# Kernel tuning notes

Hardware: AMD Instinct MI355X
Metric: run time of the kernel (lower is better)

Reference implementation:

```python
import jax, jax.numpy as jnp
import numpy as np
from jax import lax

M_RANGE = 1  # padding = m_range, kernel is (2*m_range+1)^2 = 9 classes of 3x3


def _conv(x, kernel):
    # torch F.conv2d (cross-correlation), stride 1, padding M_RANGE
    return lax.conv_general_dilated(
        x, kernel, window_strides=(1, 1),
        padding=[(M_RANGE, M_RANGE), (M_RANGE, M_RANGE)],
        dimension_numbers=('NCHW', 'OIHW', 'NCHW'))


def _construct_seg(ones, m_mask, m_kernel):
    # ones.expand_as(m_mask) * m_mask, then per-sample conv2d -> batched conv
    return _conv(ones * m_mask, m_kernel)  # [B,1,H,W]


def _construct_image(im, m_mask, appear, m_kernel):
    # im: [B,C,H,W]; m_mask: [B,K,H,W]; appear: [B,1,H,W]
    im = im * appear
    B, C, H, W = im.shape
    K = m_mask.shape[1]
    # fuse the python double loop: fold (B,C) into batch, conv K->1 once
    im_expand = (im[:, :, None, :, :] * m_mask[:, None, :, :, :]).reshape(B * C, K, H, W)
    return _conv(im_expand, m_kernel).reshape(B, C, H, W)


def setup_inputs() -> dict:
    key = jax.random.key(0)
    k0, k1, k2, k3 = jax.random.split(key, 4)
    B, C, H, W, K, N_INPUTS = 32, 3, 256, 256, 9, 2
    im_input_f = jax.random.uniform(k0, (B, N_INPUTS * C, H, W), dtype=jnp.float32)
    im_input_b = jax.random.uniform(k1, (B, N_INPUTS * C, H, W), dtype=jnp.float32)
    ones = jnp.ones((B, 1, H, W), dtype=jnp.float32)
    # gt motion masks: soft per-pixel distribution over K motion classes
    gt_motion_f = jax.nn.softmax(jax.random.normal(k2, (B, K, H, W), dtype=jnp.float32), axis=1)
    gt_motion_b = jax.nn.softmax(jax.random.normal(k3, (B, K, H, W), dtype=jnp.float32), axis=1)
    # one-hot displacement kernels: kernel i has a 1 at flat position i of the 3x3 window
    m_kernel = jnp.eye(K, dtype=jnp.float32).reshape(K, 3, 3)[None]  # [1,K,3,3]
    return {"im_input_f": im_input_f, "im_input_b": im_input_b, "ones": ones,
            "gt_motion_f": gt_motion_f, "gt_motion_b": gt_motion_b, "m_kernel": m_kernel}


def reference(im_input_f, im_input_b, ones, gt_motion_f, gt_motion_b, m_kernel):
    IM_CHANNEL = 3
    relu = jax.nn.relu
    m_mask_f, m_mask_b = gt_motion_f, gt_motion_b

    seg_f = _construct_seg(ones, m_mask_f, m_kernel)
    seg_b = _construct_seg(ones, m_mask_b, m_kernel)

    disappear_f = relu(seg_f - 1)
    appear_f = relu(1 - disappear_f)
    disappear_b = relu(seg_b - 1)
    appear_b = relu(1 - disappear_b)

    pred_f = _construct_image(im_input_f[:, -IM_CHANNEL:, :, :], m_mask_f, appear_f, m_kernel)
    pred_b = _construct_image(im_input_b[:, -IM_CHANNEL:, :, :], m_mask_b, appear_b, m_kernel)

    seg_f = 1 - relu(1 - seg_f)
    seg_b = 1 - relu(1 - seg_b)
    attn = (seg_f + 1e-5) / (seg_f + seg_b + 2e-5)  # [B,1,H,W], broadcasts over C
    pred = attn * pred_f + (1 - attn) * pred_b
    return (pred, m_mask_f, 1 - appear_f, attn, m_mask_b, 1 - appear_b, 1 - attn)
```

## Files before the change

### kernel.cpp

```cpp
#include <hip/hip_runtime.h>

#define BB 32
#define KK 9
#define CC 3
#define HH 256
#define WW 256
#define HW (HH * WW)

#define SZ_P ((size_t)BB * CC * HW)
#define SZ_M ((size_t)BB * KK * HW)
#define SZ_S ((size_t)BB * HW)

#define TX 64
#define TY 16
#define TILES_X (WW / TX)
#define TILES_Y (HH / TY)
#define TILES_PER_B (TILES_X * TILES_Y)

__global__ __launch_bounds__(256) void fused_binet_kernel(
    const float* __restrict__ im_f, const float* __restrict__ im_b,
    const float* __restrict__ gt_f, const float* __restrict__ gt_b,
    float* __restrict__ out) {
  __shared__ float s_sf[TY + 2][TX + 2];
  __shared__ float s_sb[TY + 2][TX + 2];

  int bid = blockIdx.x;
  int b = bid / TILES_PER_B;
  int t = bid % TILES_PER_B;
  int ty0 = (t / TILES_X) * TY;
  int tx0 = (t % TILES_X) * TX;

  const float* gf  = gt_f + (size_t)b * KK * HW;
  const float* gb  = gt_b + (size_t)b * KK * HW;
  const float* imf = im_f + ((size_t)b * 6 + 3) * HW;
  const float* imb = im_b + ((size_t)b * 6 + 3) * HW;

  int tid = threadIdx.x;

  for (int i = tid; i < (TY + 2) * (TX + 2); i += 256) {
    int ly = i / (TX + 2);
    int lx = i - ly * (TX + 2);
    int y = ty0 + ly - 1;
    int x = tx0 + lx - 1;
    float sf = 0.f, sb = 0.f;
    if (y >= 0 && y < HH && x >= 0 && x < WW) {
#pragma unroll
      for (int k = 0; k < KK; ++k) {
        int yy = y + (k / 3) - 1;
        int xx = x + (k % 3) - 1;
        if (yy >= 0 && yy < HH && xx >= 0 && xx < WW) {
          int off = k * HW + (yy << 8) + xx;
          sf += gf[off];
          sb += gb[off];
        }
      }
    }
    s_sf[ly][lx] = sf;
    s_sb[ly][lx] = sb;
  }
  __syncthreads();

  float* o_mf     = out + SZ_P;
  float* o_disf   = out + SZ_P + SZ_M;
  float* o_attn   = o_disf + SZ_S;
  float* o_mb     = o_attn + SZ_S;
  float* o_disb   = o_mb + SZ_M;
  float* o_1mattn = o_disb + SZ_S;

  int lx  = tid & (TX - 1);
  int ly0 = tid >> 6;

#pragma unroll
  for (int r = 0; r < 4; ++r) {
    int ly = ly0 + r * 4;
    int h = ty0 + ly;
    int w = tx0 + lx;
    int hw = (h << 8) + w;
    size_t sidx = (size_t)b * HW + hw;

    float sf = s_sf[ly + 1][lx + 1];
    float sb = s_sb[ly + 1][lx + 1];
    float dis_f = fmaxf(sf - 1.f, 0.f);
    float app_f = fmaxf(1.f - dis_f, 0.f);
    float dis_b = fmaxf(sb - 1.f, 0.f);
    float app_b = fmaxf(1.f - dis_b, 0.f);
    float sfc = 1.f - fmaxf(1.f - sf, 0.f);
    float sbc = 1.f - fmaxf(1.f - sb, 0.f);
    float attn = (sfc + 1e-5f) / (sfc + sbc + 2e-5f);

    o_disf[sidx]   = 1.f - app_f;
    o_attn[sidx]   = attn;
    o_disb[sidx]   = 1.f - app_b;
    o_1mattn[sidx] = 1.f - attn;

    float pf0 = 0.f, pf1 = 0.f, pf2 = 0.f;
    float pb0 = 0.f, pb1 = 0.f, pb2 = 0.f;
#pragma unroll
    for (int k = 0; k < KK; ++k) {
      size_t moff = (size_t)b * KK * HW + (size_t)k * HW + hw;
      o_mf[moff] = gf[k * HW + hw];
      o_mb[moff] = gb[k * HW + hw];

      int y = h + (k / 3) - 1;
      int x = w + (k % 3) - 1;
      if (y >= 0 && y < HH && x >= 0 && x < WW) {
        int p = (y << 8) + x;
        float sfq = s_sf[ly + (k / 3)][lx + (k % 3)];
        float af = fmaxf(1.f - fmaxf(sfq - 1.f, 0.f), 0.f);
        float cf = af * gf[k * HW + p];
        pf0 = fmaf(cf, imf[p], pf0);
        pf1 = fmaf(cf, imf[HW + p], pf1);
        pf2 = fmaf(cf, imf[2 * HW + p], pf2);
        float sbq = s_sb[ly + (k / 3)][lx + (k % 3)];
        float ab = fmaxf(1.f - fmaxf(sbq - 1.f, 0.f), 0.f);
        float cb = ab * gb[k * HW + p];
        pb0 = fmaf(cb, imb[p], pb0);
        pb1 = fmaf(cb, imb[HW + p], pb1);
        pb2 = fmaf(cb, imb[2 * HW + p], pb2);
      }
    }
    float at2 = 1.f - attn;
    size_t pbase = (size_t)b * CC * HW + hw;
    out[pbase]          = fmaf(attn, pf0, at2 * pb0);
    out[pbase + HW]     = fmaf(attn, pf1, at2 * pb1);
    out[pbase + 2 * HW] = fmaf(attn, pf2, at2 * pb2);
  }
}

extern "C" void kernel_launch(void* const* d_in, const int* in_sizes, int n_in,
                              void* d_out, int out_size, void* d_ws, size_t ws_size,
                              hipStream_t stream) {
  const float* im_f = (const float*)d_in[0];
  const float* im_b = (const float*)d_in[1];
  const float* gt_f = (const float*)d_in[3];
  const float* gt_b = (const float*)d_in[4];
  float* out = (float*)d_out;

  dim3 block(256);
  dim3 grid(BB * TILES_PER_B);

  fused_binet_kernel<<<grid, block, 0, stream>>>(im_f, im_b, gt_f, gt_b, out);
}
```

Before: 458.0 us.

## Compute seg in registers per pixel, halo-only ring pass, swizzle block order

Each thread now loads the 9 shifted mask values for its own pixels once, keeps them in registers to form the seg sum and later reuse it for the image prediction, and writes the interior of the shared seg tile directly. A separate pass computes only the halo ring. Block size goes to 512 threads with 2 rows per thread, and block indices are remapped with an XCD-style swizzle so neighbouring tiles share L2. The aim is to cut the redundant gathers of the mask tensor, at the cost of higher register pressure from the 36 kept values.

Measured after the change: 421.0 us. 1.09x faster.

```diff
diff --git a/kernel.cpp b/kernel.cpp
--- a/kernel.cpp
+++ b/kernel.cpp
@@ -13,11 +13,9 @@
 
 #define TX 64
 #define TY 16
-#define TILES_X (WW / TX)
-#define TILES_Y (HH / TY)
-#define TILES_PER_B (TILES_X * TILES_Y)
+#define RING ((TY + 2) * (TX + 2) - TY * TX)
 
-__global__ __launch_bounds__(256) void fused_binet_kernel(
+__global__ __launch_bounds__(512) void fused_binet_kernel(
     const float* __restrict__ im_f, const float* __restrict__ im_b,
     const float* __restrict__ gt_f, const float* __restrict__ gt_b,
     float* __restrict__ out) {
@@ -25,40 +23,16 @@
   __shared__ float s_sb[TY + 2][TX + 2];
 
   int bid = blockIdx.x;
-  int b = bid / TILES_PER_B;
-  int t = bid % TILES_PER_B;
-  int ty0 = (t / TILES_X) * TY;
-  int tx0 = (t % TILES_X) * TX;
+  int actual = ((bid & 7) << 8) | (bid >> 3);
+  int b   = actual >> 6;
+  int rem = actual & 63;
+  int tx0 = (rem >> 4) << 6;
+  int ty0 = (rem & 15) << 4;
 
   const float* gf  = gt_f + (size_t)b * KK * HW;
   const float* gb  = gt_b + (size_t)b * KK * HW;
   const float* imf = im_f + ((size_t)b * 6 + 3) * HW;
   const float* imb = im_b + ((size_t)b * 6 + 3) * HW;
-
-  int tid = threadIdx.x;
-
-  for (int i = tid; i < (TY + 2) * (TX + 2); i += 256) {
-    int ly = i / (TX + 2);
-    int lx = i - ly * (TX + 2);
-    int y = ty0 + ly - 1;
-    int x = tx0 + lx - 1;
-    float sf = 0.f, sb = 0.f;
-    if (y >= 0 && y < HH && x >= 0 && x < WW) {
-#pragma unroll
-      for (int k = 0; k < KK; ++k) {
-        int yy = y + (k / 3) - 1;
-        int xx = x + (k % 3) - 1;
-        if (yy >= 0 && yy < HH && xx >= 0 && xx < WW) {
-          int off = k * HW + (yy << 8) + xx;
-          sf += gf[off];
-          sb += gb[off];
-        }
-      }
-    }
-    s_sf[ly][lx] = sf;
-    s_sb[ly][lx] = sb;
-  }
-  __syncthreads();
 
   float* o_mf     = out + SZ_P;
   float* o_disf   = out + SZ_P + SZ_M;
@@ -67,19 +41,83 @@
   float* o_disb   = o_mb + SZ_M;
   float* o_1mattn = o_disb + SZ_S;
 
+  int tid = threadIdx.x;
   int lx  = tid & (TX - 1);
   int ly0 = tid >> 6;
 
+  float rf[2][KK], rb[2][KK];
+  float segf[2], segb[2];
+
 #pragma unroll
-  for (int r = 0; r < 4; ++r) {
-    int ly = ly0 + r * 4;
-    int h = ty0 + ly;
-    int w = tx0 + lx;
-    int hw = (h << 8) + w;
+  for (int r = 0; r < 2; ++r) {
+    int ly = ly0 + r * 8;
+    int h  = ty0 + ly;
+    int w  = tx0 + lx;
+    int hw = (h << 8) | w;
+    float sf = 0.f, sb = 0.f;
+#pragma unroll
+    for (int k = 0; k < KK; ++k) {
+      int y = h + (k / 3) - 1;
+      int x = w + (k % 3) - 1;
+      float vf = 0.f, vb = 0.f;
+      if ((unsigned)y < HH && (unsigned)x < WW) {
+        int p = k * HW + (y << 8) + x;
+        vf = gf[p];
+        vb = gb[p];
+      }
+      rf[r][k] = vf;
+      rb[r][k] = vb;
+      sf += vf;
+      sb += vb;
+      size_t moff = (size_t)b * KK * HW + (size_t)k * HW + hw;
+      o_mf[moff] = gf[k * HW + hw];
+      o_mb[moff] = gb[k * HW + hw];
+    }
+    segf[r] = sf;
+    segb[r] = sb;
+    s_sf[ly + 1][lx + 1] = sf;
+    s_sb[ly + 1][lx + 1] = sb;
+  }
+
+  if (tid < RING) {
+    int ly, lxr;
+    if (tid < TX + 2) { ly = 0; lxr = tid; }
+    else if (tid < 2 * (TX + 2)) { ly = TY + 1; lxr = tid - (TX + 2); }
+    else {
+      int j = tid - 2 * (TX + 2);
+      ly  = 1 + (j & 15);
+      lxr = (j >> 4) ? (TX + 1) : 0;
+    }
+    int yq = ty0 + ly - 1;
+    int xq = tx0 + lxr - 1;
+    float sf = 0.f, sb = 0.f;
+    if ((unsigned)yq < HH && (unsigned)xq < WW) {
+#pragma unroll
+      for (int k = 0; k < KK; ++k) {
+        int y = yq + (k / 3) - 1;
+        int x = xq + (k % 3) - 1;
+        if ((unsigned)y < HH && (unsigned)x < WW) {
+          int p = k * HW + (y << 8) + x;
+          sf += gf[p];
+          sb += gb[p];
+        }
+      }
+    }
+    s_sf[ly][lxr] = sf;
+    s_sb[ly][lxr] = sb;
+  }
+  __syncthreads();
+
+#pragma unroll
+  for (int r = 0; r < 2; ++r) {
+    int ly = ly0 + r * 8;
+    int h  = ty0 + ly;
+    int w  = tx0 + lx;
+    int hw = (h << 8) | w;
     size_t sidx = (size_t)b * HW + hw;
 
-    float sf = s_sf[ly + 1][lx + 1];
-    float sb = s_sb[ly + 1][lx + 1];
+    float sf = segf[r];
+    float sb = segb[r];
     float dis_f = fmaxf(sf - 1.f, 0.f);
     float app_f = fmaxf(1.f - dis_f, 0.f);
     float dis_b = fmaxf(sb - 1.f, 0.f);
@@ -97,23 +135,20 @@
     float pb0 = 0.f, pb1 = 0.f, pb2 = 0.f;
 #pragma unroll
     for (int k = 0; k < KK; ++k) {
-      size_t moff = (size_t)b * KK * HW + (size_t)k * HW + hw;
-      o_mf[moff] = gf[k * HW + hw];
-      o_mb[moff] = gb[k * HW + hw];
-
-      int y = h + (k / 3) - 1;
-      int x = w + (k % 3) - 1;
-      if (y >= 0 && y < HH && x >= 0 && x < WW) {
+      int dy = k / 3, dx = k % 3;
+      int y = h + dy - 1;
+      int x = w + dx - 1;
+      if ((unsigned)y < HH && (unsigned)x < WW) {
         int p = (y << 8) + x;
-        float sfq = s_sf[ly + (k / 3)][lx + (k % 3)];
-        float af = fmaxf(1.f - fmaxf(sfq - 1.f, 0.f), 0.f);
-        float cf = af * gf[k * HW + p];
+        float sfq = s_sf[ly + dy][lx + dx];
+        float af  = fmaxf(1.f - fmaxf(sfq - 1.f, 0.f), 0.f);
+        float cf  = af * rf[r][k];
         pf0 = fmaf(cf, imf[p], pf0);
         pf1 = fmaf(cf, imf[HW + p], pf1);
         pf2 = fmaf(cf, imf[2 * HW + p], pf2);
-        float sbq = s_sb[ly + (k / 3)][lx + (k % 3)];
-        float ab = fmaxf(1.f - fmaxf(sbq - 1.f, 0.f), 0.f);
-        float cb = ab * gb[k * HW + p];
+        float sbq = s_sb[ly + dy][lx + dx];
+        float ab  = fmaxf(1.f - fmaxf(sbq - 1.f, 0.f), 0.f);
+        float cb  = ab * rb[r][k];
         pb0 = fmaf(cb, imb[p], pb0);
         pb1 = fmaf(cb, imb[HW + p], pb1);
         pb2 = fmaf(cb, imb[2 * HW + p], pb2);
@@ -136,8 +171,8 @@
   const float* gt_b = (const float*)d_in[4];
   float* out = (float*)d_out;
 
-  dim3 block(256);
-  dim3 grid(BB * TILES_PER_B);
+  dim3 block(512);
+  dim3 grid(BB * 64);
 
   fused_binet_kernel<<<grid, block, 0, stream>>>(im_f, im_b, gt_f, gt_b, out);
 }
```
